# Performance work log

Hardware: AMD Instinct MI355X
Metric: run time of the kernel (lower is better)

## Reference

```python
import jax, jax.numpy as jnp
import numpy as np

N_NODES = 10000
N_EDGES = 160000
DIM = 512
LN_EPS = 1e-5


def setup_inputs() -> dict:
    key = jax.random.key(0)
    ks = jax.random.split(key, 6)
    scale = 1.0 / np.sqrt(DIM)
    h = jax.random.normal(ks[0], (N_NODES, DIM), dtype=jnp.float32)
    edge_index = jax.random.randint(ks[1], (2, N_EDGES), 0, N_NODES, dtype=jnp.int32)
    W_self = jax.random.normal(ks[2], (DIM, DIM), dtype=jnp.float32) * scale
    b_self = jnp.zeros((DIM,), dtype=jnp.float32)
    W_neigh = jax.random.normal(ks[3], (DIM, DIM), dtype=jnp.float32) * scale
    b_neigh = jnp.zeros((DIM,), dtype=jnp.float32)
    ln_gamma = jnp.ones((DIM,), dtype=jnp.float32)
    ln_beta = jnp.zeros((DIM,), dtype=jnp.float32)
    return {"h": h, "edge_index": edge_index, "W_self": W_self, "b_self": b_self,
            "W_neigh": W_neigh, "b_neigh": b_neigh, "ln_gamma": ln_gamma, "ln_beta": ln_beta}


def reference(h, edge_index, W_self, b_self, W_neigh, b_neigh, ln_gamma, ln_beta):
    n = h.shape[0]
    src = edge_index[0]
    dst = edge_index[1]
    # per-edge message: gather dst features, dense linear (torch Linear => x @ W.T + b)
    msg = h[dst] @ W_neigh.T + b_neigh            # [E, dim]
    # scatter-add aggregate into src nodes
    neigh = jax.ops.segment_sum(msg, src, num_segments=n)            # [N, dim]
    deg = jax.ops.segment_sum(jnp.ones(src.shape, h.dtype), src, num_segments=n)
    deg = jnp.maximum(deg, 1.0)
    neigh = neigh / deg[:, None]
    # self transform + relu (dropout is identity in eval)
    out = jax.nn.relu(h @ W_self.T + b_self + neigh)
    # residual LayerNorm
    x = h + out
    mean = jnp.mean(x, axis=-1, keepdims=True)
    var = jnp.mean(jnp.square(x - mean), axis=-1, keepdims=True)
    return (x - mean) * jax.lax.rsqrt(var + LN_EPS) * ln_gamma + ln_beta
```

## Files before the change

### kernel.cpp

```cpp
#include <hip/hip_runtime.h>

#define N_NODES 10000
#define N_PAD   10048
#define N_EDGES 160000
#define DIM     512
#define KDIM    1024
#define CAP     64

#define BM 64
#define BN 128
#define BK 64
#define KITERS (KDIM / BK)

typedef __attribute__((ext_vector_type(8))) short bf16x8;
typedef __attribute__((ext_vector_type(4))) float f32x4;

static __device__ __forceinline__ ushort f2bf(float f) {
    union { float f; unsigned u; } x; x.f = f;
    unsigned u = x.u + 0x7fff + ((x.u >> 16) & 1);
    return (ushort)(u >> 16);
}
static __device__ __forceinline__ float b2f(ushort u) {
    union { unsigned u; float f; } x; x.u = ((unsigned)u) << 16; return x.f;
}

__global__ __launch_bounds__(256) void conv_w(
    const float* __restrict__ Wself, const float* __restrict__ Wneigh,
    ushort* __restrict__ Wc, int* __restrict__ cnt)
{
    int idx = blockIdx.x * 256 + threadIdx.x;
    if (idx < N_NODES) cnt[idx] = 0;
    int c  = idx >> 7;
    int k8 = idx & 127;
    const float* src = (k8 < 64) ? (Wself + (size_t)c * DIM + k8 * 8)
                                 : (Wneigh + (size_t)c * DIM + (k8 - 64) * 8);
    float4 v0 = *(const float4*)src;
    float4 v1 = *(const float4*)(src + 4);
    ushort* dst = Wc + (size_t)c * KDIM + k8 * 8;
    ushort4 o0 = { f2bf(v0.x), f2bf(v0.y), f2bf(v0.z), f2bf(v0.w) };
    ushort4 o1 = { f2bf(v1.x), f2bf(v1.y), f2bf(v1.z), f2bf(v1.w) };
    *(ushort4*)dst = o0;
    *(ushort4*)(dst + 4) = o1;
}

__global__ __launch_bounds__(256) void conv_x(
    const float* __restrict__ h, ushort* __restrict__ X,
    const int* __restrict__ eidx, int* __restrict__ cnt, int* __restrict__ col)
{
    int idx = blockIdx.x * 256 + threadIdx.x;
    if (idx < N_EDGES) {
        int s = eidx[idx];
        int d = eidx[N_EDGES + idx];
        int p = atomicAdd(&cnt[s], 1);
        if (p < CAP) col[(s << 6) + p] = d;
    }
    int n  = idx >> 7;
    int k8 = idx & 127;
    if (n >= N_PAD) return;
    ushort* dst = X + (size_t)n * KDIM + k8 * 8;
    if (n >= N_NODES) {
        ushort4 z = {0, 0, 0, 0};
        *(ushort4*)dst = z;
        *(ushort4*)(dst + 4) = z;
        return;
    }
    if (k8 >= 64) return;
    const float* src = h + (size_t)n * DIM + k8 * 8;
    float4 v0 = *(const float4*)src;
    float4 v1 = *(const float4*)(src + 4);
    ushort4 o0 = { f2bf(v0.x), f2bf(v0.y), f2bf(v0.z), f2bf(v0.w) };
    ushort4 o1 = { f2bf(v1.x), f2bf(v1.y), f2bf(v1.z), f2bf(v1.w) };
    *(ushort4*)dst = o0;
    *(ushort4*)(dst + 4) = o1;
}

__global__ __launch_bounds__(256) void gather_agg(
    const int* __restrict__ cnt, const int* __restrict__ col,
    ushort* __restrict__ X, float* __restrict__ deg)
{
    int gid  = blockIdx.x * 256 + threadIdx.x;
    int n    = gid >> 6;
    int lane = gid & 63;
    if (n >= N_NODES) return;
    int d  = cnt[n];
    int nk = d < CAP ? d : CAP;

    int myc = (lane < nk) ? col[(n << 6) + lane] : 0;

    float s0 = 0.f, s1 = 0.f, s2 = 0.f, s3 = 0.f;
    float s4 = 0.f, s5 = 0.f, s6 = 0.f, s7 = 0.f;
    int k = 0;
    for (; k + 8 <= nk; k += 8) {
        bf16x8 v[8];
#pragma unroll
        for (int u = 0; u < 8; ++u) {
            int dst = __shfl(myc, k + u);
            v[u] = *(const bf16x8*)(X + (size_t)dst * KDIM + lane * 8);
        }
#pragma unroll
        for (int u = 0; u < 8; ++u) {
            s0 += b2f((ushort)v[u][0]); s1 += b2f((ushort)v[u][1]);
            s2 += b2f((ushort)v[u][2]); s3 += b2f((ushort)v[u][3]);
            s4 += b2f((ushort)v[u][4]); s5 += b2f((ushort)v[u][5]);
            s6 += b2f((ushort)v[u][6]); s7 += b2f((ushort)v[u][7]);
        }
    }
    for (; k < nk; ++k) {
        int dst = __shfl(myc, k);
        bf16x8 v = *(const bf16x8*)(X + (size_t)dst * KDIM + lane * 8);
        s0 += b2f((ushort)v[0]); s1 += b2f((ushort)v[1]);
        s2 += b2f((ushort)v[2]); s3 += b2f((ushort)v[3]);
        s4 += b2f((ushort)v[4]); s5 += b2f((ushort)v[5]);
        s6 += b2f((ushort)v[6]); s7 += b2f((ushort)v[7]);
    }
    float inv = 1.0f / fmaxf((float)d, 1.0f);
    ushort* xr = X + (size_t)n * KDIM + DIM + lane * 8;
    ushort4 o0 = { f2bf(s0 * inv), f2bf(s1 * inv), f2bf(s2 * inv), f2bf(s3 * inv) };
    ushort4 o1 = { f2bf(s4 * inv), f2bf(s5 * inv), f2bf(s6 * inv), f2bf(s7 * inv) };
    *(ushort4*)xr       = o0;
    *(ushort4*)(xr + 4) = o1;
    if (lane == 0) deg[n] = (float)d;
}

#define MFMA(A, B, C) __builtin_amdgcn_mfma_f32_16x16x32_bf16(A, B, C, 0, 0, 0)

__global__ __launch_bounds__(128) void mfma_gemm(
    const ushort* __restrict__ X, const ushort* __restrict__ Wc,
    const float* __restrict__ deg,
    const float* __restrict__ bself, const float* __restrict__ bneigh,
    ushort* __restrict__ Y)
{
    __shared__ ushort As[2][BM * BK];
    __shared__ ushort Bs[2][BN * BK];
    __shared__ float  hb_s[BM];

    const int t    = threadIdx.x;
    const int lane = t & 63;
    const int wave = t >> 6;
    const int row0 = blockIdx.y * BM;
    const int col0 = blockIdx.x * BN;
    const int wc   = wave * 64;
    const int fr   = lane & 15;
    const int fq   = lane >> 4;

    if (t < BM) {
        int n = row0 + t;
        hb_s[t] = (n < N_NODES && deg[n] > 0.0f) ? 1.0f : 0.0f;
    }

#define STAGE(BUF, IT)                                                         \
    {                                                                          \
        const int k0s = (IT) * BK;                                             \
        _Pragma("unroll")                                                      \
        for (int s = 0; s < 4; ++s) {                                          \
            int c = t + s * 128;                                               \
            int row = c >> 3;                                                  \
            int ks = k0s + (((c & 7) ^ (row & 7)) << 3);                       \
            __builtin_amdgcn_global_load_lds(                                  \
                (const __attribute__((address_space(1))) void*)                \
                    (X + (size_t)(row0 + row) * KDIM + ks),                    \
                (__attribute__((address_space(3))) void*)(&As[BUF][c * 8]),    \
                16, 0, 0);                                                     \
        }                                                                      \
        _Pragma("unroll")                                                      \
        for (int s = 0; s < 8; ++s) {                                          \
            int c = t + s * 128;                                               \
            int row = c >> 3;                                                  \
            int ks = k0s + (((c & 7) ^ (row & 7)) << 3);                       \
            __builtin_amdgcn_global_load_lds(                                  \
                (const __attribute__((address_space(1))) void*)                \
                    (Wc + (size_t)(col0 + row) * KDIM + ks),                   \
                (__attribute__((address_space(3))) void*)(&Bs[BUF][c * 8]),    \
                16, 0, 0);                                                     \
        }                                                                      \
    }

    f32x4 acc[4][4];
#pragma unroll
    for (int i = 0; i < 4; ++i)
#pragma unroll
        for (int j = 0; j < 4; ++j) acc[i][j] = (f32x4){0.f, 0.f, 0.f, 0.f};

    STAGE(0, 0);
    __syncthreads();

    int buf = 0;
    for (int it = 0; it < KITERS; ++it) {
        if (it + 1 < KITERS) STAGE(buf ^ 1, it + 1);

        const ushort* as = As[buf];
        const ushort* bs = Bs[buf];
#pragma unroll
        for (int inner = 0; inner < 2; ++inner) {
            const int sw = (((inner * 4 + fq) ^ (fr & 7)) << 3);
            bf16x8 a[4], b[4];
#pragma unroll
            for (int i = 0; i < 4; ++i)
                a[i] = *(const bf16x8*)(as + (i * 16 + fr) * BK + sw);
#pragma unroll
            for (int j = 0; j < 4; ++j)
                b[j] = *(const bf16x8*)(bs + (wc + j * 16 + fr) * BK + sw);
#pragma unroll
            for (int i = 0; i < 4; ++i)
#pragma unroll
                for (int j = 0; j < 4; ++j)
                    acc[i][j] = MFMA(a[i], b[j], acc[i][j]);
        }
        __syncthreads();
        buf ^= 1;
    }

#pragma unroll
    for (int i = 0; i < 4; ++i) {
#pragma unroll
        for (int r = 0; r < 4; ++r) {
            int lr = i * 16 + fq * 4 + r;
            int gr = row0 + lr;
            float hb = hb_s[lr];
            ushort* yrow = Y + (size_t)gr * DIM;
#pragma unroll
            for (int j = 0; j < 4; ++j) {
                int gc = col0 + wc + j * 16 + fr;
                float v = fmaxf(acc[i][j][r] + bself[gc] + hb * bneigh[gc], 0.f);
                yrow[gc] = f2bf(v);
            }
        }
    }
}

__global__ __launch_bounds__(256) void ln_kernel(
    const ushort* __restrict__ Y, const float* __restrict__ h,
    const float* __restrict__ g, const float* __restrict__ b,
    float* __restrict__ out)
{
    __shared__ float red[8];
    int n = blockIdx.x;
    int t = threadIdx.x;
    float2 hv = *(const float2*)(h + (size_t)n * DIM + t * 2);
    ushort2 yv = *(const ushort2*)(Y + (size_t)n * DIM + t * 2);
    float v0 = hv.x + b2f(yv.x);
    float v1 = hv.y + b2f(yv.y);
    float s  = v0 + v1;
    float sq = v0 * v0 + v1 * v1;
#pragma unroll
    for (int off = 32; off >= 1; off >>= 1) {
        s  += __shfl_xor(s, off);
        sq += __shfl_xor(sq, off);
    }
    int wave = t >> 6;
    if ((t & 63) == 0) { red[wave] = s; red[4 + wave] = sq; }
    __syncthreads();
    s  = red[0] + red[1] + red[2] + red[3];
    sq = red[4] + red[5] + red[6] + red[7];
    float mean = s * (1.0f / DIM);
    float var  = sq * (1.0f / DIM) - mean * mean;
    float rstd = rsqrtf(var + 1e-5f);
    float2 gv = *(const float2*)(g + t * 2);
    float2 bv = *(const float2*)(b + t * 2);
    float2 o;
    o.x = (v0 - mean) * rstd * gv.x + bv.x;
    o.y = (v1 - mean) * rstd * gv.y + bv.y;
    *(float2*)(out + (size_t)n * DIM + t * 2) = o;
}

extern "C" void kernel_launch(void* const* d_in, const int* in_sizes, int n_in,
                              void* d_out, int out_size, void* d_ws, size_t ws_size,
                              hipStream_t stream)
{
    const float* h      = (const float*)d_in[0];
    const int*   eidx   = (const int*)d_in[1];
    const float* Wself  = (const float*)d_in[2];
    const float* bself  = (const float*)d_in[3];
    const float* Wneigh = (const float*)d_in[4];
    const float* bneigh = (const float*)d_in[5];
    const float* gamma  = (const float*)d_in[6];
    const float* beta   = (const float*)d_in[7];
    float* out = (float*)d_out;

    ushort* X   = (ushort*)d_ws;
    ushort* Wc  = X + (size_t)N_PAD * KDIM;
    ushort* Y   = Wc + (size_t)DIM * KDIM;
    float* deg  = (float*)(Y + (size_t)N_PAD * DIM);
    int* cnt    = (int*)(deg + N_NODES);
    int* col    = cnt + N_NODES;

    conv_w<<<(DIM * 128) / 256, 256, 0, stream>>>(Wself, Wneigh, Wc, cnt);
    conv_x<<<(N_PAD * 128) / 256, 256, 0, stream>>>(h, X, eidx, cnt, col);
    gather_agg<<<(N_NODES * 64) / 256, 256, 0, stream>>>(cnt, col, X, deg);

    dim3 gg(DIM / BN, N_PAD / BM);
    mfma_gemm<<<gg, 128, 0, stream>>>(X, Wc, deg, bself, bneigh, Y);

    ln_kernel<<<N_NODES, 256, 0, stream>>>(Y, h, gamma, beta, out);
}
```

Measured before the change: 82.60 us.

## Gather neighbors from fp8 copy of h and enlarge GEMM tile to 128x128

conv_x now also writes an fp8 (e4m3) copy of h. gather_agg reads these 8-byte rows and decodes them with packed fp8-to-f32 conversions, which halves the bytes moved in the bandwidth-bound neighbor gather. Separately, the GEMM grows to a 128x128 tile with 256 threads in a 2x2 wave layout and pads N to 10112; per-row degree flags are read from global memory instead of shared memory. The fp8 gather loses precision, which risks exceeding the accuracy tolerance, and the larger tile cuts the number of blocks from 628 to 316, leaving a partial wave on 256 CUs.

Result: no change. 81.44 us (-1.4%).

```diff
diff --git a/kernel.cpp b/kernel.cpp
--- a/kernel.cpp
+++ b/kernel.cpp
@@ -1,19 +1,20 @@
 #include <hip/hip_runtime.h>
 
 #define N_NODES 10000
-#define N_PAD   10048
+#define N_PAD   10112
 #define N_EDGES 160000
 #define DIM     512
 #define KDIM    1024
 #define CAP     64
 
-#define BM 64
+#define BM 128
 #define BN 128
 #define BK 64
 #define KITERS (KDIM / BK)
 
 typedef __attribute__((ext_vector_type(8))) short bf16x8;
 typedef __attribute__((ext_vector_type(4))) float f32x4;
+typedef __attribute__((ext_vector_type(2))) float f32x2;
 
 static __device__ __forceinline__ ushort f2bf(float f) {
     union { float f; unsigned u; } x; x.f = f;
@@ -45,6 +46,7 @@
 
 __global__ __launch_bounds__(256) void conv_x(
     const float* __restrict__ h, ushort* __restrict__ X,
+    unsigned char* __restrict__ H8,
     const int* __restrict__ eidx, int* __restrict__ cnt, int* __restrict__ col)
 {
     int idx = blockIdx.x * 256 + threadIdx.x;
@@ -72,10 +74,20 @@
     ushort4 o1 = { f2bf(v1.x), f2bf(v1.y), f2bf(v1.z), f2bf(v1.w) };
     *(ushort4*)dst = o0;
     *(ushort4*)(dst + 4) = o1;
+    uint2 p8;
+    int r0 = 0, r1 = 0;
+    r0 = __builtin_amdgcn_cvt_pk_fp8_f32(v0.x, v0.y, r0, false);
+    r0 = __builtin_amdgcn_cvt_pk_fp8_f32(v0.z, v0.w, r0, true);
+    r1 = __builtin_amdgcn_cvt_pk_fp8_f32(v1.x, v1.y, r1, false);
+    r1 = __builtin_amdgcn_cvt_pk_fp8_f32(v1.z, v1.w, r1, true);
+    p8.x = (unsigned)r0;
+    p8.y = (unsigned)r1;
+    *(uint2*)(H8 + (size_t)n * DIM + k8 * 8) = p8;
 }
 
 __global__ __launch_bounds__(256) void gather_agg(
     const int* __restrict__ cnt, const int* __restrict__ col,
+    const unsigned char* __restrict__ H8,
     ushort* __restrict__ X, float* __restrict__ deg)
 {
     int gid  = blockIdx.x * 256 + threadIdx.x;
@@ -87,36 +99,38 @@
 
     int myc = (lane < nk) ? col[(n << 6) + lane] : 0;
 
-    float s0 = 0.f, s1 = 0.f, s2 = 0.f, s3 = 0.f;
-    float s4 = 0.f, s5 = 0.f, s6 = 0.f, s7 = 0.f;
+    f32x2 a01 = {0.f, 0.f}, a23 = {0.f, 0.f}, a45 = {0.f, 0.f}, a67 = {0.f, 0.f};
     int k = 0;
     for (; k + 8 <= nk; k += 8) {
-        bf16x8 v[8];
+        uint2 v[8];
 #pragma unroll
         for (int u = 0; u < 8; ++u) {
             int dst = __shfl(myc, k + u);
-            v[u] = *(const bf16x8*)(X + (size_t)dst * KDIM + lane * 8);
+            v[u] = *(const uint2*)(H8 + (size_t)dst * DIM + lane * 8);
         }
 #pragma unroll
         for (int u = 0; u < 8; ++u) {
-            s0 += b2f((ushort)v[u][0]); s1 += b2f((ushort)v[u][1]);
-            s2 += b2f((ushort)v[u][2]); s3 += b2f((ushort)v[u][3]);
-            s4 += b2f((ushort)v[u][4]); s5 += b2f((ushort)v[u][5]);
-            s6 += b2f((ushort)v[u][6]); s7 += b2f((ushort)v[u][7]);
+            f32x2 d01 = __builtin_amdgcn_cvt_pk_f32_fp8((int)v[u].x, false);
+            f32x2 d23 = __builtin_amdgcn_cvt_pk_f32_fp8((int)v[u].x, true);
+            f32x2 d45 = __builtin_amdgcn_cvt_pk_f32_fp8((int)v[u].y, false);
+            f32x2 d67 = __builtin_amdgcn_cvt_pk_f32_fp8((int)v[u].y, true);
+            a01 += d01; a23 += d23; a45 += d45; a67 += d67;
         }
     }
     for (; k < nk; ++k) {
         int dst = __shfl(myc, k);
-        bf16x8 v = *(const bf16x8*)(X + (size_t)dst * KDIM + lane * 8);
-        s0 += b2f((ushort)v[0]); s1 += b2f((ushort)v[1]);
-        s2 += b2f((ushort)v[2]); s3 += b2f((ushort)v[3]);
-        s4 += b2f((ushort)v[4]); s5 += b2f((ushort)v[5]);
-        s6 += b2f((ushort)v[6]); s7 += b2f((ushort)v[7]);
+        uint2 v = *(const uint2*)(H8 + (size_t)dst * DIM + lane * 8);
+        a01 += __builtin_amdgcn_cvt_pk_f32_fp8((int)v.x, false);
+        a23 += __builtin_amdgcn_cvt_pk_f32_fp8((int)v.x, true);
+        a45 += __builtin_amdgcn_cvt_pk_f32_fp8((int)v.y, false);
+        a67 += __builtin_amdgcn_cvt_pk_f32_fp8((int)v.y, true);
     }
     float inv = 1.0f / fmaxf((float)d, 1.0f);
     ushort* xr = X + (size_t)n * KDIM + DIM + lane * 8;
-    ushort4 o0 = { f2bf(s0 * inv), f2bf(s1 * inv), f2bf(s2 * inv), f2bf(s3 * inv) };
-    ushort4 o1 = { f2bf(s4 * inv), f2bf(s5 * inv), f2bf(s6 * inv), f2bf(s7 * inv) };
+    ushort4 o0 = { f2bf(a01[0] * inv), f2bf(a01[1] * inv),
+                   f2bf(a23[0] * inv), f2bf(a23[1] * inv) };
+    ushort4 o1 = { f2bf(a45[0] * inv), f2bf(a45[1] * inv),
+                   f2bf(a67[0] * inv), f2bf(a67[1] * inv) };
     *(ushort4*)xr       = o0;
     *(ushort4*)(xr + 4) = o1;
     if (lane == 0) deg[n] = (float)d;
@@ -124,7 +138,7 @@
 
 #define MFMA(A, B, C) __builtin_amdgcn_mfma_f32_16x16x32_bf16(A, B, C, 0, 0, 0)
 
-__global__ __launch_bounds__(128) void mfma_gemm(
+__global__ __launch_bounds__(256) void mfma_gemm(
     const ushort* __restrict__ X, const ushort* __restrict__ Wc,
     const float* __restrict__ deg,
     const float* __restrict__ bself, const float* __restrict__ bneigh,
@@ -132,28 +146,23 @@
 {
     __shared__ ushort As[2][BM * BK];
     __shared__ ushort Bs[2][BN * BK];
-    __shared__ float  hb_s[BM];
 
     const int t    = threadIdx.x;
     const int lane = t & 63;
     const int wave = t >> 6;
     const int row0 = blockIdx.y * BM;
     const int col0 = blockIdx.x * BN;
-    const int wc   = wave * 64;
+    const int wr   = (wave >> 1) * 64;
+    const int wc   = (wave & 1) * 64;
     const int fr   = lane & 15;
     const int fq   = lane >> 4;
-
-    if (t < BM) {
-        int n = row0 + t;
-        hb_s[t] = (n < N_NODES && deg[n] > 0.0f) ? 1.0f : 0.0f;
-    }
 
 #define STAGE(BUF, IT)                                                         \
     {                                                                          \
         const int k0s = (IT) * BK;                                             \
         _Pragma("unroll")                                                      \
         for (int s = 0; s < 4; ++s) {                                          \
-            int c = t + s * 128;                                               \
+            int c = t + s * 256;                                               \
             int row = c >> 3;                                                  \
             int ks = k0s + (((c & 7) ^ (row & 7)) << 3);                       \
             __builtin_amdgcn_global_load_lds(                                  \
@@ -163,8 +172,8 @@
                 16, 0, 0);                                                     \
         }                                                                      \
         _Pragma("unroll")                                                      \
-        for (int s = 0; s < 8; ++s) {                                          \
-            int c = t + s * 128;                                               \
+        for (int s = 0; s < 4; ++s) {                                          \
+            int c = t + s * 256;                                               \
             int row = c >> 3;                                                  \
             int ks = k0s + (((c & 7) ^ (row & 7)) << 3);                       \
             __builtin_amdgcn_global_load_lds(                                  \
@@ -196,7 +205,7 @@
             bf16x8 a[4], b[4];
 #pragma unroll
             for (int i = 0; i < 4; ++i)
-                a[i] = *(const bf16x8*)(as + (i * 16 + fr) * BK + sw);
+                a[i] = *(const bf16x8*)(as + (wr + i * 16 + fr) * BK + sw);
 #pragma unroll
             for (int j = 0; j < 4; ++j)
                 b[j] = *(const bf16x8*)(bs + (wc + j * 16 + fr) * BK + sw);
@@ -214,9 +223,8 @@
     for (int i = 0; i < 4; ++i) {
 #pragma unroll
         for (int r = 0; r < 4; ++r) {
-            int lr = i * 16 + fq * 4 + r;
-            int gr = row0 + lr;
-            float hb = hb_s[lr];
+            int gr = row0 + wr + i * 16 + fq * 4 + r;
+            float hb = (gr < N_NODES && deg[gr] > 0.0f) ? 1.0f : 0.0f;
             ushort* yrow = Y + (size_t)gr * DIM;
 #pragma unroll
             for (int j = 0; j < 4; ++j) {
@@ -283,13 +291,14 @@
     float* deg  = (float*)(Y + (size_t)N_PAD * DIM);
     int* cnt    = (int*)(deg + N_NODES);
     int* col    = cnt + N_NODES;
+    unsigned char* H8 = (unsigned char*)(col + (size_t)N_NODES * CAP);
 
     conv_w<<<(DIM * 128) / 256, 256, 0, stream>>>(Wself, Wneigh, Wc, cnt);
-    conv_x<<<(N_PAD * 128) / 256, 256, 0, stream>>>(h, X, eidx, cnt, col);
-    gather_agg<<<(N_NODES * 64) / 256, 256, 0, stream>>>(cnt, col, X, deg);
+    conv_x<<<(N_PAD * 128) / 256, 256, 0, stream>>>(h, X, H8, eidx, cnt, col);
+    gather_agg<<<(N_NODES * 64) / 256, 256, 0, stream>>>(cnt, col, H8, X, deg);
 
     dim3 gg(DIM / BN, N_PAD / BM);
-    mfma_gemm<<<gg, 128, 0, stream>>>(X, Wc, deg, bself, bneigh, Y);
+    mfma_gemm<<<gg, 256, 0, stream>>>(X, Wc, deg, bself, bneigh, Y);
 
     ln_kernel<<<N_NODES, 256, 0, stream>>>(Y, h, gamma, beta, out);
 }
```
